# Performance work log

Hardware: AMD Instinct MI355X
Metric: run time of the kernel (lower is better)

## Reference

```python
import jax, jax.numpy as jnp
import numpy as np


def setup_inputs() -> dict:
    key = jax.random.key(0)
    ks = jax.random.split(key, 7)
    B, D, d1, d2, d3 = 256, 256, 1024, 512, 256
    s = lambda f: 1.0 / np.sqrt(f)  # torch nn.Linear-style init scale
    return {
        "x": jax.random.normal(ks[0], (B, D), jnp.float32),
        "W1": jax.random.normal(ks[1], (d1, D), jnp.float32) * s(D),
        "b1": jax.random.normal(ks[2], (d1,), jnp.float32) * s(D),
        "W2": jax.random.normal(ks[3], (d2, d1), jnp.float32) * s(d1),
        "b2": jax.random.normal(ks[4], (d2,), jnp.float32) * s(d1),
        "W3": jax.random.normal(ks[5], (d3, d2), jnp.float32) * s(d2),
        "b3": jax.random.normal(ks[6], (d3,), jnp.float32) * s(d2),
        "k": 10,
    }


def _border_dists(x, W1, b1, W2, b2, W3, b3):
    # Layer 1: pre-activations and boundary distances. For the first layer the
    # effective linear map is W1 itself (shared across the batch).
    z1 = x @ W1.T + b1                                   # [B, d1]
    dist1 = jnp.abs(z1) / jnp.linalg.norm(W1, axis=1)    # [B, d1]
    m1 = (z1 > 0).astype(x.dtype)
    V1 = m1[:, :, None] * W1[None]                       # [B, d1, D] per-instance map after ReLU
    h1 = m1 * z1

    # Layer 2
    z2 = h1 @ W2.T + b2                                  # [B, d2]
    V2 = jnp.einsum('oi,bid->bod', W2, V1)               # [B, d2, D]
    dist2 = jnp.abs(z2) / jnp.linalg.norm(V2, axis=2)
    m2 = (z2 > 0).astype(x.dtype)
    h2 = m2 * z2

    # Layer 3
    z3 = h2 @ W3.T + b3                                  # [B, d3]
    V3 = jnp.einsum('oi,bid->bod', W3, m2[:, :, None] * V2)  # [B, d3, D]
    dist3 = jnp.abs(z3) / jnp.linalg.norm(V3, axis=2)

    return jnp.concatenate([dist1, dist2, dist3], axis=1)  # [B, d1+d2+d3]


def reference(x, W1, b1, W2, b2, W3, b3, k):
    dists = _border_dists(x, W1, b1, W2, b2, W3, b3)
    # smallest-k distances per instance via top_k on negated distances
    neg_top, _ = jax.lax.top_k(-dists, k)                # [B, k]
    return jnp.sum(-neg_top)                             # border-distance loss (scalar)
```

## Files before the change

kernel.cpp:

```cpp
#include <hip/hip_runtime.h>
#include <math.h>
#include <float.h>

#define B   256
#define D   256
#define D1  1024
#define D2  512
#define D3  256
#define NDIST (D1 + D2 + D3)
#define CQ  2.0f

typedef __attribute__((ext_vector_type(8))) short short8;
typedef __attribute__((ext_vector_type(4))) float f32x4;
typedef __attribute__((ext_vector_type(4))) int   i32x4;

__device__ __forceinline__ float waveReduceSum(float v) {
    #pragma unroll
    for (int off = 32; off > 0; off >>= 1)
        v += __shfl_down(v, off, 64);
    return v;
}
__device__ __forceinline__ float waveReduceMax(float v) {
    #pragma unroll
    for (int off = 32; off > 0; off >>= 1)
        v = fmaxf(v, __shfl_down(v, off, 64));
    return v;
}
__device__ __forceinline__ unsigned short f2bf(float f) {
    unsigned int u = __float_as_uint(f);
    u = (u + 0x7FFFu + ((u >> 16) & 1u)) >> 16;
    return (unsigned short)u;
}
__device__ __forceinline__ float bf2f(unsigned short h) {
    return __uint_as_float(((unsigned int)h) << 16);
}
__device__ __forceinline__ void gld16(const void* g, void* l) {
    __builtin_amdgcn_global_load_lds(
        (const __attribute__((address_space(1))) unsigned int*)g,
        (__attribute__((address_space(3))) unsigned int*)l, 16, 0, 0);
}
__device__ __forceinline__ int swz_src(int row, int lane) {
    return ((lane & 3) + ((row >> 1) & 3)) & 3;
}
__device__ __forceinline__ int swz_frag(int row, int quad) {
    return row * 32 + (((quad - ((row >> 1) & 3)) & 3) * 8);
}

__device__ __forceinline__ void split8(const float* p, short8& h8, short8& l8) {
    float4 a = *(const float4*)(p);
    float4 b = *(const float4*)(p + 4);
    float hv[8] = { a.x, a.y, a.z, a.w, b.x, b.y, b.z, b.w };
    #pragma unroll
    for (int q = 0; q < 8; q++) {
        unsigned short hh = f2bf(hv[q]);
        h8[q] = (short)hh;
        l8[q] = (short)f2bf(hv[q] - bf2f(hh));
    }
}

template <int KD, int KL>
__device__ __forceinline__ void mfma3_64(
    const unsigned short* __restrict__ Ahi, const unsigned short* __restrict__ Alo,
    const unsigned short* __restrict__ Bhi, const unsigned short* __restrict__ Blo,
    int m0, int n0, int k0, unsigned short* sm, f32x4 acc[2][2]) {
    int tid = threadIdx.x;
    int l = tid & 63, w = tid >> 6;
    int rsub = l >> 2;
    int quad = l >> 4, l16 = l & 15;
    int wm = (w >> 1) * 32, wn = (w & 1) * 32;
    unsigned short* sAh = sm;
    unsigned short* sAl = sm + 2048;
    unsigned short* sBh = sm + 4096;
    unsigned short* sBl = sm + 6144;
    ptrdiff_t dA = Alo - Ahi, dB = Blo - Bhi;
    int rloc = w * 16 + rsub;
    int c = swz_src(rloc, l);
    const unsigned short* pa = Ahi + (size_t)(m0 + rloc) * KD + k0 + c * 8;
    const unsigned short* pb = Bhi + (size_t)(n0 + rloc) * KD + k0 + c * 8;
    int aoff[2], boff[2];
    #pragma unroll
    for (int mt = 0; mt < 2; mt++) aoff[mt] = swz_frag(wm + mt * 16 + l16, quad);
    #pragma unroll
    for (int nt = 0; nt < 2; nt++) boff[nt] = swz_frag(wn + nt * 16 + l16, quad);
    for (int kk = 0; kk < KL; kk += 32) {
        gld16(pa + kk,      sAh + w * 512);
        gld16(pa + dA + kk, sAl + w * 512);
        gld16(pb + kk,      sBh + w * 512);
        gld16(pb + dB + kk, sBl + w * 512);
        __syncthreads();
        short8 ah[2], al[2], bh[2], bl[2];
        #pragma unroll
        for (int mt = 0; mt < 2; mt++) {
            ah[mt] = *(const short8*)(sAh + aoff[mt]);
            al[mt] = *(const short8*)(sAl + aoff[mt]);
        }
        #pragma unroll
        for (int nt = 0; nt < 2; nt++) {
            bh[nt] = *(const short8*)(sBh + boff[nt]);
            bl[nt] = *(const short8*)(sBl + boff[nt]);
        }
        #pragma unroll
        for (int mt = 0; mt < 2; mt++)
            #pragma unroll
            for (int nt = 0; nt < 2; nt++) {
                acc[mt][nt] = __builtin_amdgcn_mfma_f32_16x16x32_bf16(ah[mt], bh[nt], acc[mt][nt], 0, 0, 0);
                acc[mt][nt] = __builtin_amdgcn_mfma_f32_16x16x32_bf16(ah[mt], bl[nt], acc[mt][nt], 0, 0, 0);
                acc[mt][nt] = __builtin_amdgcn_mfma_f32_16x16x32_bf16(al[mt], bh[nt], acc[mt][nt], 0, 0, 0);
            }
        __syncthreads();
    }
}

__global__ __launch_bounds__(256) void k_l1p(
    const float* __restrict__ x, const float* __restrict__ W1,
    const float* __restrict__ W2, const float* __restrict__ W3,
    const float* __restrict__ b1,
    float* __restrict__ dists, unsigned char* __restrict__ m1q,
    unsigned short* __restrict__ h1hi, unsigned short* __restrict__ h1lo,
    float* __restrict__ zeros, float* __restrict__ outp,
    unsigned short* __restrict__ W2hi, unsigned short* __restrict__ W2lo,
    unsigned short* __restrict__ W3hi, unsigned short* __restrict__ W3lo,
    signed char* __restrict__ W1Ti8, float* __restrict__ saq,
    signed char* __restrict__ W2i8,  float* __restrict__ sbq,
    signed char* __restrict__ W3i8,  float* __restrict__ s3q,
    float* __restrict__ rn1) {
    __shared__ __align__(16) unsigned short sm[8192];
    int blk = blockIdx.x;
    int t = threadIdx.x;

    if (blk < 64) {
        unsigned short* sAh = sm;
        unsigned short* sAl = sm + 2048;
        unsigned short* sBh = sm + 4096;
        unsigned short* sBl = sm + 6144;
        int m0 = (blk & 3) * 64, n0 = (blk >> 2) * 64;
        int l = t & 63, w = t >> 6;
        int rsub = l >> 2;
        int quad = l >> 4, l16 = l & 15;
        int wm = (w >> 1) * 32, wn = (w & 1) * 32;
        int rloc = w * 16 + rsub;
        int c = swz_src(rloc, l);
        const float* pax = x + (size_t)(m0 + rloc) * D + c * 8;
        const float* pbw = W1 + (size_t)(n0 + rloc) * D + c * 8;
        int aoff[2], boff[2];
        #pragma unroll
        for (int mt = 0; mt < 2; mt++) aoff[mt] = swz_frag(wm + mt * 16 + l16, quad);
        #pragma unroll
        for (int nt = 0; nt < 2; nt++) boff[nt] = swz_frag(wn + nt * 16 + l16, quad);
        int wrA = w * 512 + l * 8;
        f32x4 acc[2][2] = {};
        for (int kk = 0; kk < D; kk += 32) {
            short8 ha, la, hb, lb;
            split8(pax + kk, ha, la);
            split8(pbw + kk, hb, lb);
            *(short8*)(sAh + wrA) = ha;
            *(short8*)(sAl + wrA) = la;
            *(short8*)(sBh + wrA) = hb;
            *(short8*)(sBl + wrA) = lb;
            __syncthreads();
            short8 ah[2], al[2], bh[2], bl[2];
            #pragma unroll
            for (int mt = 0; mt < 2; mt++) {
                ah[mt] = *(const short8*)(sAh + aoff[mt]);
                al[mt] = *(const short8*)(sAl + aoff[mt]);
            }
            #pragma unroll
            for (int nt = 0; nt < 2; nt++) {
                bh[nt] = *(const short8*)(sBh + boff[nt]);
                bl[nt] = *(const short8*)(sBl + boff[nt]);
            }
            #pragma unroll
            for (int mt = 0; mt < 2; mt++)
                #pragma unroll
                for (int nt = 0; nt < 2; nt++) {
                    acc[mt][nt] = __builtin_amdgcn_mfma_f32_16x16x32_bf16(ah[mt], bh[nt], acc[mt][nt], 0, 0, 0);
                    acc[mt][nt] = __builtin_amdgcn_mfma_f32_16x16x32_bf16(ah[mt], bl[nt], acc[mt][nt], 0, 0, 0);
                    acc[mt][nt] = __builtin_amdgcn_mfma_f32_16x16x32_bf16(al[mt], bh[nt], acc[mt][nt], 0, 0, 0);
                }
            __syncthreads();
        }
        #pragma unroll
        for (int mt = 0; mt < 2; mt++)
            #pragma unroll
            for (int nt = 0; nt < 2; nt++) {
                int n = n0 + wn + nt * 16 + l16;
                float bv = b1[n];
                #pragma unroll
                for (int r = 0; r < 4; r++) {
                    int m = m0 + wm + mt * 16 + quad * 4 + r;
                    float z = acc[mt][nt][r] + bv;
                    size_t idx = (size_t)m * D1 + n;
                    dists[idx] = fabsf(z);
                    m1q[idx] = (z > 0.f) ? 0xFFu : 0u;
                    float h = z > 0.f ? z : 0.f;
                    unsigned short hh = f2bf(h);
                    h1hi[idx] = hh;
                    h1lo[idx] = f2bf(h - bf2f(hh));
                }
            }
        return;
    }
    if (blk < 448) {
        if (blk == 64 && t == 0) outp[0] = 0.f;
        int i4 = (blk - 64) * 1024 + t * 4;
        *(float4*)(zeros + i4) = make_float4(0.f, 0.f, 0.f, 0.f);
        return;
    }
    if (blk < 480) {
        int ty = t >> 5, tx = t & 31;
        int d = (blk - 448) * 8 + ty;
        float m = 0.f;
        for (int i = tx; i < D1; i += 32) m = fmaxf(m, fabsf(W1[(size_t)i * D + d]));
        #pragma unroll
        for (int off = 16; off > 0; off >>= 1) m = fmaxf(m, __shfl_down(m, off, 32));
        m = __shfl(m, 0, 32);
        m = fmaxf(m, 1e-20f);
        if (tx == 0) saq[d] = m / 127.f;
        float inv = 127.f / m;
        for (int i = tx; i < D1; i += 32) {
            int q = __float2int_rn(W1[(size_t)i * D + d] * inv);
            W1Ti8[(size_t)d * D1 + i] = (signed char)q;
        }
        return;
    }
    if (blk < 608) {
        int o = (blk - 480) * 4 + (t >> 6);
        int l = t & 63;
        const float* row = W2 + (size_t)o * D1;
        float4 v[4];
        #pragma unroll
        for (int jj = 0; jj < 4; jj++) v[jj] = *(const float4*)(row + jj * 256 + l * 4);
        float m = 0.f;
        #pragma unroll
        for (int jj = 0; jj < 4; jj++)
            m = fmaxf(m, fmaxf(fmaxf(fabsf(v[jj].x), fabsf(v[jj].y)),
                               fmaxf(fabsf(v[jj].z), fabsf(v[jj].w))));
        m = waveReduceMax(m);
        m = __shfl(m, 0, 64);
        m = fmaxf(m, 1e-20f);
        if (l == 0) sbq[o] = m / 127.f;
        float inv = 127.f / m;
        #pragma unroll
        for (int jj = 0; jj < 4; jj++) {
            int base = jj * 256 + l * 4;
            int q0 = __float2int_rn(v[jj].x * inv);
            int q1 = __float2int_rn(v[jj].y * inv);
            int q2 = __float2int_rn(v[jj].z * inv);
            int q3 = __float2int_rn(v[jj].w * inv);
            unsigned int pk = (unsigned)(q0 & 255) | ((unsigned)(q1 & 255) << 8) |
                              ((unsigned)(q2 & 255) << 16) | ((unsigned)(q3 & 255) << 24);
            *(unsigned int*)(W2i8 + (size_t)o * D1 + base) = pk;
            ushort4 h, lo;
            h.x = f2bf(v[jj].x); lo.x = f2bf(v[jj].x - bf2f(h.x));
            h.y = f2bf(v[jj].y); lo.y = f2bf(v[jj].y - bf2f(h.y));
            h.z = f2bf(v[jj].z); lo.z = f2bf(v[jj].z - bf2f(h.z));
            h.w = f2bf(v[jj].w); lo.w = f2bf(v[jj].w - bf2f(h.w));
            *(ushort4*)(W2hi + (size_t)o * D1 + base) = h;
            *(ushort4*)(W2lo + (size_t)o * D1 + base) = lo;
        }
        return;
    }
    if (blk < 672) {
        int p = (blk - 608) * 4 + (t >> 6);
        int l = t & 63;
        const float* row = W3 + (size_t)p * D2;
        float4 v[2];
        #pragma unroll
        for (int jj = 0; jj < 2; jj++) v[jj] = *(const float4*)(row + jj * 256 + l * 4);
        float m = 0.f;
        #pragma unroll
        for (int jj = 0; jj < 2; jj++)
            m = fmaxf(m, fmaxf(fmaxf(fabsf(v[jj].x), fabsf(v[jj].y)),
                               fmaxf(fabsf(v[jj].z), fabsf(v[jj].w))));
        m = waveReduceMax(m);
        m = __shfl(m, 0, 64);
        m = fmaxf(m, 1e-20f);
        if (l == 0) s3q[p] = m / 127.f;
        float inv = 127.f / m;
        #pragma unroll
        for (int jj = 0; jj < 2; jj++) {
            int base = jj * 256 + l * 4;
            int q0 = __float2int_rn(v[jj].x * inv);
            int q1 = __float2int_rn(v[jj].y * inv);
            int q2 = __float2int_rn(v[jj].z * inv);
            int q3 = __float2int_rn(v[jj].w * inv);
            unsigned int pk = (unsigned)(q0 & 255) | ((unsigned)(q1 & 255) << 8) |
                              ((unsigned)(q2 & 255) << 16) | ((unsigned)(q3 & 255) << 24);
            *(unsigned int*)(W3i8 + (size_t)p * D2 + base) = pk;
            ushort4 h, lo;
            h.x = f2bf(v[jj].x); lo.x = f2bf(v[jj].x - bf2f(h.x));
            h.y = f2bf(v[jj].y); lo.y = f2bf(v[jj].y - bf2f(h.y));
            h.z = f2bf(v[jj].z); lo.z = f2bf(v[jj].z - bf2f(h.z));
            h.w = f2bf(v[jj].w); lo.w = f2bf(v[jj].w - bf2f(h.w));
            *(ushort4*)(W3hi + (size_t)p * D2 + base) = h;
            *(ushort4*)(W3lo + (size_t)p * D2 + base) = lo;
        }
        return;
    }
    {
        int gw = (blk - 672) * 4 + (t >> 6);
        int lane = t & 63;
        const float* row = W1 + (size_t)gw * D;
        float s = 0.f;
        for (int tt = lane; tt < D; tt += 64) { float v = row[tt]; s += v * v; }
        s = waveReduceSum(s);
        if (lane == 0) rn1[gw] = sqrtf(s);
    }
}

__global__ __launch_bounds__(256, 2) void k_big1(
    const unsigned short* __restrict__ h1hi, const unsigned short* __restrict__ h1lo,
    const unsigned short* __restrict__ W2hi, const unsigned short* __restrict__ W2lo,
    float* __restrict__ z2,
    const signed char* __restrict__ W1Ti8,
    const signed char* __restrict__ W2i8,
    const unsigned char* __restrict__ m1q,
    const float* __restrict__ saq,
    const float* __restrict__ sbq,
    signed char* __restrict__ qV2,
    float* __restrict__ norm2) {
    __shared__ __align__(16) unsigned char smem[67584];
    int bid = blockIdx.x;

    if (bid < 128) {
        unsigned short* sm = (unsigned short*)smem;
        int m0 = (bid & 3) * 64, n0 = ((bid >> 2) & 7) * 64, k0 = (bid >> 5) * 256;
        f32x4 acc[2][2] = {};
        mfma3_64<D1, 256>(h1hi, h1lo, W2hi, W2lo, m0, n0, k0, sm, acc);
        int l = threadIdx.x & 63, w = threadIdx.x >> 6;
        int quad = l >> 4, l16 = l & 15;
        int wm = (w >> 1) * 32, wn = (w & 1) * 32;
        #pragma unroll
        for (int mt = 0; mt < 2; mt++)
            #pragma unroll
            for (int nt = 0; nt < 2; nt++) {
                int n = n0 + wn + nt * 16 + l16;
                #pragma unroll
                for (int r = 0; r < 4; r++) {
                    int m = m0 + wm + mt * 16 + quad * 4 + r;
                    atomicAdd(&z2[(size_t)m * D2 + n], acc[mt][nt][r]);
                }
            }
        return;
    }

    int j = bid - 128;
    int m0 = (j & 1) * 128;
    int o0 = ((j >> 1) & 3) * 128;
    int b0 = (j >> 3) * 2;
    int tid = threadIdx.x;
    int l = tid & 63, w = tid >> 6;
    int quad = l >> 4, l16 = l & 15;
    int wm = (w >> 1) * 64, wn = (w & 1) * 64;
    unsigned char* mbuf = (unsigned char*)smem + 65536;

    *(int2*)(mbuf + tid * 8) = *(const int2*)(m1q + (size_t)b0 * D1 + tid * 8);

    const signed char* pa[4];
    const signed char* pb[4];
    int lrow = l >> 3, ls = l & 7;
    #pragma unroll
    for (int r = 0; r < 4; r++) {
        int row = r * 32 + w * 8 + lrow;
        int c = (ls + (row & 7)) & 7;
        pa[r] = W1Ti8 + (size_t)(m0 + row) * D1 + c * 16;
        pb[r] = W2i8 + (size_t)(o0 + row) * D1 + c * 16;
    }
    int aoff[4][2], boff[4][2];
    #pragma unroll
    for (int mt = 0; mt < 4; mt++) {
        int tr = wm + mt * 16 + l16;
        #pragma unroll
        for (int ks = 0; ks < 2; ks++)
            aoff[mt][ks] = tr * 128 + (((ks * 4 + quad) - (tr & 7)) & 7) * 16;
    }
    #pragma unroll
    for (int nt = 0; nt < 4; nt++) {
        int tr = wn + nt * 16 + l16;
        #pragma unroll
        for (int ks = 0; ks < 2; ks++)
            boff[nt][ks] = tr * 128 + (((ks * 4 + quad) - (tr & 7)) & 7) * 16;
    }

    i32x4 acc[2][4][4];
    #pragma unroll
    for (int g = 0; g < 2; g++)
        #pragma unroll
        for (int i = 0; i < 4; i++)
            #pragma unroll
            for (int jj = 0; jj < 4; jj++) acc[g][i][jj] = (i32x4)0;

    int wr = w * 1024 + l * 16;
    i32x4 sga[4], sgb[4];
    #pragma unroll
    for (int r = 0; r < 4; r++) {
        sga[r] = *(const i32x4*)(pa[r]);
        sgb[r] = *(const i32x4*)(pb[r]);
    }
    {
        signed char* buf0 = (signed char*)smem;
        #pragma unroll
        for (int r = 0; r < 4; r++) {
            *(i32x4*)(buf0 + r * 4096 + wr) = sga[r];
            *(i32x4*)(buf0 + 16384 + r * 4096 + wr) = sgb[r];
        }
    }
    __syncthreads();

    #pragma unroll
    for (int t = 0; t < 8; t++) {
        const signed char* bufc = (const signed char*)smem + ((t & 1) << 15);
        signed char* bufn = (signed char*)smem + (((t + 1) & 1) << 15);
        if (t < 7) {
            int kn = (t + 1) * 128;
            #pragma unroll
            for (int r = 0; r < 4; r++) {
                sga[r] = *(const i32x4*)(pa[r] + kn);
                sgb[r] = *(const i32x4*)(pb[r] + kn);
            }
        }
        const signed char* As = bufc;
        const signed char* Bs = bufc + 16384;
        #pragma unroll
        for (int ks = 0; ks < 2; ks++) {
            i32x4 mva = *(const i32x4*)(mbuf +        t * 128 + ks * 64 + quad * 16);
            i32x4 mvb = *(const i32x4*)(mbuf + 1024 + t * 128 + ks * 64 + quad * 16);
            i32x4 a[4], bq[4];
            #pragma unroll
            for (int mt = 0; mt < 4; mt++)
                a[mt] = *(const i32x4*)(As + aoff[mt][ks]);
            #pragma unroll
            for (int nt = 0; nt < 4; nt++)
                bq[nt] = *(const i32x4*)(Bs + boff[nt][ks]);
            #pragma unroll
            for (int mt = 0; mt < 4; mt++) {
                i32x4 a0 = a[mt] & mva;
                i32x4 a1 = a[mt] & mvb;
                #pragma unroll
                for (int nt = 0; nt < 4; nt++)
                    acc[0][mt][nt] = __builtin_amdgcn_mfma_i32_16x16x64_i8(
                        a0, bq[nt], acc[0][mt][nt], 0, 0, 0);
                #pragma unroll
                for (int nt = 0; nt < 4; nt++)
                    acc[1][mt][nt] = __builtin_amdgcn_mfma_i32_16x16x64_i8(
                        a1, bq[nt], acc[1][mt][nt], 0, 0, 0);
            }
        }
        if (t < 7) {
            #pragma unroll
            for (int r = 0; r < 4; r++) {
                *(i32x4*)(bufn + r * 4096 + wr) = sga[r];
                *(i32x4*)(bufn + 16384 + r * 4096 + wr) = sgb[r];
            }
        }
        __syncthreads();
    }

    float sad[4][4];
    #pragma unroll
    for (int mt = 0; mt < 4; mt++)
        #pragma unroll
        for (int r = 0; r < 4; r++)
            sad[mt][r] = saq[m0 + wm + mt * 16 + quad * 4 + r];
    float sbv[4], sbdq[4];
    #pragma unroll
    for (int nt = 0; nt < 4; nt++) {
        sbv[nt] = sbq[o0 + wn + nt * 16 + l16];
        sbdq[nt] = sbv[nt] * (1.0f / CQ);
    }

    #pragma unroll
    for (int g = 0; g < 2; g++) {
        int bg = b0 + g;
        float nrm[4] = {0.f, 0.f, 0.f, 0.f};
        signed char* qb = qV2 + (size_t)bg * (D * D2);
        #pragma unroll
        for (int mt = 0; mt < 4; mt++) {
            int dbase = m0 + wm + mt * 16 + quad * 4;
            #pragma unroll
            for (int r = 0; r < 4; r++) {
                float sa = sad[mt][r];
                size_t rowoff = (size_t)(dbase + r) * D2;
                #pragma unroll
                for (int nt = 0; nt < 4; nt++) {
                    float tv = (float)acc[g][mt][nt][r];
                    float u = tv * sa;
                    nrm[nt] = fmaf(u, u, nrm[nt]);
                    int qi = __float2int_rn(tv * sbdq[nt]);
                    qi = max(-127, min(127, qi));
                    qb[rowoff + o0 + wn + nt * 16 + l16] = (signed char)qi;
                }
            }
        }
        #pragma unroll
        for (int nt = 0; nt < 4; nt++) {
            float s = nrm[nt] * (sbv[nt] * sbv[nt]);
            s += __shfl_down(s, 32, 64);
            s += __shfl_down(s, 16, 64);
            if (l < 16)
                atomicAdd(&norm2[(size_t)bg * D2 + o0 + wn + nt * 16 + l], s);
        }
    }
}

__global__ __launch_bounds__(256, 2) void k_big2(
    const float* __restrict__ z2,
    const float* __restrict__ b2,
    const unsigned short* __restrict__ W3hi, const unsigned short* __restrict__ W3lo,
    float* __restrict__ z3,
    const signed char* __restrict__ W3i8,
    const signed char* __restrict__ qV2,
    const float* __restrict__ saq,
    const float* __restrict__ s3q,
    float* __restrict__ norm3) {
    __shared__ __align__(16) unsigned char smem[66048];
    int bid = blockIdx.x;
    int tid = threadIdx.x;

    if (bid < 32) {
        unsigned short* sAh = (unsigned short*)smem;
        unsigned short* sAl = sAh + 2048;
        unsigned short* sBh = sAh + 4096;
        unsigned short* sBl = sAh + 6144;
        int m0 = (bid & 3) * 64, n0 = ((bid >> 2) & 3) * 64, k0 = (bid >> 4) * 256;
        int l = tid & 63, w = tid >> 6;
        int rsub = l >> 2;
        int quad = l >> 4, l16 = l & 15;
        int wm = (w >> 1) * 32, wn = (w & 1) * 32;
        int rloc = w * 16 + rsub;
        int c = swz_src(rloc, l);
        const float* pz  = z2 + (size_t)(m0 + rloc) * D2 + k0 + c * 8;
        const float* pbi = b2 + k0 + c * 8;
        const unsigned short* pb = W3hi + (size_t)(n0 + rloc) * D2 + k0 + c * 8;
        ptrdiff_t dB = W3lo - W3hi;
        int aoff[2], boff[2];
        #pragma unroll
        for (int mt = 0; mt < 2; mt++) aoff[mt] = swz_frag(wm + mt * 16 + l16, quad);
        #pragma unroll
        for (int nt = 0; nt < 2; nt++) boff[nt] = swz_frag(wn + nt * 16 + l16, quad);
        int wrA = w * 512 + l * 8;
        f32x4 acc[2][2] = {};
        for (int kk = 0; kk < 256; kk += 32) {
            gld16(pb + kk,      sBh + w * 512);
            gld16(pb + dB + kk, sBl + w * 512);
            float4 za = *(const float4*)(pz + kk);
            float4 zb = *(const float4*)(pz + kk + 4);
            float4 ba = *(const float4*)(pbi + kk);
            float4 bb = *(const float4*)(pbi + kk + 4);
            float hv[8] = { za.x + ba.x, za.y + ba.y, za.z + ba.z, za.w + ba.w,
                            zb.x + bb.x, zb.y + bb.y, zb.z + bb.z, zb.w + bb.w };
            short8 h8, l8;
            #pragma unroll
            for (int q2 = 0; q2 < 8; q2++) {
                float h = hv[q2] > 0.f ? hv[q2] : 0.f;
                unsigned short hh = f2bf(h);
                h8[q2] = (short)hh;
                l8[q2] = (short)f2bf(h - bf2f(hh));
            }
            *(short8*)(sAh + wrA) = h8;
            *(short8*)(sAl + wrA) = l8;
            __syncthreads();
            short8 ah[2], al[2], bh[2], bl[2];
            #pragma unroll
            for (int mt = 0; mt < 2; mt++) {
                ah[mt] = *(const short8*)(sAh + aoff[mt]);
                al[mt] = *(const short8*)(sAl + aoff[mt]);
            }
            #pragma unroll
            for (int nt = 0; nt < 2; nt++) {
                bh[nt] = *(const short8*)(sBh + boff[nt]);
                bl[nt] = *(const short8*)(sBl + boff[nt]);
            }
            #pragma unroll
            for (int mt = 0; mt < 2; mt++)
                #pragma unroll
                for (int nt = 0; nt < 2; nt++) {
                    acc[mt][nt] = __builtin_amdgcn_mfma_f32_16x16x32_bf16(ah[mt], bh[nt], acc[mt][nt], 0, 0, 0);
                    acc[mt][nt] = __builtin_amdgcn_mfma_f32_16x16x32_bf16(ah[mt], bl[nt], acc[mt][nt], 0, 0, 0);
                    acc[mt][nt] = __builtin_amdgcn_mfma_f32_16x16x32_bf16(al[mt], bh[nt], acc[mt][nt], 0, 0, 0);
                }
            __syncthreads();
        }
        #pragma unroll
        for (int mt = 0; mt < 2; mt++)
            #pragma unroll
            for (int nt = 0; nt < 2; nt++) {
                int n = n0 + wn + nt * 16 + l16;
                #pragma unroll
                for (int r = 0; r < 4; r++) {
                    int m = m0 + wm + mt * 16 + quad * 4 + r;
                    atomicAdd(&z3[(size_t)m * D3 + n], acc[mt][nt][r]);
                }
            }
        return;
    }

    int j = bid - 32;
    unsigned char* mbuf = (unsigned char*)smem + 65536;
    int m0 = (j & 1) * 128;
    int n0 = ((j >> 1) & 1) * 128;
    int bc = j >> 2;
    int l = tid & 63, w = tid >> 6;
    int quad = l >> 4, l16 = l & 15;
    int wm = (w >> 1) * 64, wn = (w & 1) * 64;
    const signed char* Bsrc = qV2 + (size_t)bc * (D * D2);

    {
        #pragma unroll
        for (int rr = 0; rr < 2; rr++) {
            int o = tid * 2 + rr;
            float z = z2[(size_t)bc * D2 + o] + b2[o];
            mbuf[o] = (z > 0.f) ? 0xFFu : 0u;
        }
    }

    const signed char* pa[4];
    const signed char* pb[4];
    int lrow = l >> 3, ls = l & 7;
    #pragma unroll
    for (int r = 0; r < 4; r++) {
        int row = r * 32 + w * 8 + lrow;
        int c = (ls + (row & 7)) & 7;
        pa[r] = W3i8 + (size_t)(m0 + row) * D2 + c * 16;
        pb[r] = Bsrc + (size_t)(n0 + row) * D2 + c * 16;
    }
    int aoff[4][2], boff[4][2];
    #pragma unroll
    for (int mt = 0; mt < 4; mt++) {
        int tr = wm + mt * 16 + l16;
        #pragma unroll
        for (int ks = 0; ks < 2; ks++)
            aoff[mt][ks] = tr * 128 + (((ks * 4 + quad) - (tr & 7)) & 7) * 16;
    }
    #pragma unroll
    for (int nt = 0; nt < 4; nt++) {
        int tr = wn + nt * 16 + l16;
        #pragma unroll
        for (int ks = 0; ks < 2; ks++)
            boff[nt][ks] = tr * 128 + (((ks * 4 + quad) - (tr & 7)) & 7) * 16;
    }

    i32x4 acc[4][4];
    #pragma unroll
    for (int i = 0; i < 4; i++)
        #pragma unroll
        for (int jj = 0; jj < 4; jj++) acc[i][jj] = (i32x4)0;

    int wr = w * 1024 + l * 16;
    i32x4 sga[4], sgb[4];
    #pragma unroll
    for (int r = 0; r < 4; r++) {
        sga[r] = *(const i32x4*)(pa[r]);
        sgb[r] = *(const i32x4*)(pb[r]);
    }
    {
        signed char* buf0 = (signed char*)smem;
        #pragma unroll
        for (int r = 0; r < 4; r++) {
            *(i32x4*)(buf0 + r * 4096 + wr) = sga[r];
            *(i32x4*)(buf0 + 16384 + r * 4096 + wr) = sgb[r];
        }
    }
    __syncthreads();

    #pragma unroll
    for (int t = 0; t < 4; t++) {
        const signed char* bufc = (const signed char*)smem + ((t & 1) << 15);
        signed char* bufn = (signed char*)smem + (((t + 1) & 1) << 15);
        if (t < 3) {
            int kn = (t + 1) * 128;
            #pragma unroll
            for (int r = 0; r < 4; r++) {
                sga[r] = *(const i32x4*)(pa[r] + kn);
                sgb[r] = *(const i32x4*)(pb[r] + kn);
            }
        }
        int kk = t * 128;
        const signed char* As = bufc;
        const signed char* Bs = bufc + 16384;
        i32x4 mv0 = *(const i32x4*)(mbuf + kk + quad * 16);
        i32x4 mv1 = *(const i32x4*)(mbuf + kk + 64 + quad * 16);
        #pragma unroll
        for (int ks = 0; ks < 2; ks++) {
            i32x4 mv = ks ? mv1 : mv0;
            i32x4 a[4], bq[4];
            #pragma unroll
            for (int mt = 0; mt < 4; mt++)
                a[mt] = *(const i32x4*)(As + aoff[mt][ks]);
            #pragma unroll
            for (int nt = 0; nt < 4; nt++)
                bq[nt] = (*(const i32x4*)(Bs + boff[nt][ks])) & mv;
            #pragma unroll
            for (int mt = 0; mt < 4; mt++)
                #pragma unroll
                for (int nt = 0; nt < 4; nt++)
                    acc[mt][nt] = __builtin_amdgcn_mfma_i32_16x16x64_i8(
                        a[mt], bq[nt], acc[mt][nt], 0, 0, 0);
        }
        if (t < 3) {
            #pragma unroll
            for (int r = 0; r < 4; r++) {
                *(i32x4*)(bufn + r * 4096 + wr) = sga[r];
                *(i32x4*)(bufn + 16384 + r * 4096 + wr) = sgb[r];
            }
        }
        __syncthreads();
    }

    float saCQ[4];
    #pragma unroll
    for (int nt = 0; nt < 4; nt++)
        saCQ[nt] = saq[n0 + wn + nt * 16 + l16] * CQ;

    #pragma unroll
    for (int mt = 0; mt < 4; mt++)
        #pragma unroll
        for (int r = 0; r < 4; r++) {
            float s = 0.f;
            #pragma unroll
            for (int nt = 0; nt < 4; nt++) {
                float v = (float)acc[mt][nt][r] * saCQ[nt];
                s += v * v;
            }
            s += __shfl_down(s, 8, 64);
            s += __shfl_down(s, 4, 64);
            s += __shfl_down(s, 2, 64);
            s += __shfl_down(s, 1, 64);
            if (l16 == 0) {
                int p = m0 + wm + mt * 16 + quad * 4 + r;
                float s3 = s3q[p];
                atomicAdd(&norm3[(size_t)bc * D3 + p], s * s3 * s3);
            }
        }
}

__global__ __launch_bounds__(256) void k_topk(
    const float* __restrict__ dists,
    const float* __restrict__ rn1,
    const float* __restrict__ z2, const float* __restrict__ b2,
    const float* __restrict__ norm2,
    const float* __restrict__ z3, const float* __restrict__ b3,
    const float* __restrict__ norm3,
    const int* __restrict__ kp, float* __restrict__ outp) {
    int t = threadIdx.x;
    int wv = t >> 6, lane = t & 63;
    int b = blockIdx.x * 4 + wv;
    float lv[28];
    #pragma unroll
    for (int j = 0; j < 16; j++) {
        int n = lane + 64 * j;
        lv[j] = dists[(size_t)b * D1 + n] / rn1[n];
    }
    #pragma unroll
    for (int j = 16; j < 24; j++) {
        int o = lane + 64 * (j - 16);
        float zz = z2[(size_t)b * D2 + o] + b2[o];
        lv[j] = fabsf(zz) / sqrtf(norm2[(size_t)b * D2 + o]);
    }
    #pragma unroll
    for (int j = 24; j < 28; j++) {
        int p = lane + 64 * (j - 24);
        float zz = z3[(size_t)b * D3 + p] + b3[p];
        lv[j] = fabsf(zz) / sqrtf(norm3[(size_t)b * D3 + p]);
    }
    int k = *kp;
    if (k > NDIST) k = NDIST;
    float sum = 0.f;
    for (int it = 0; it < k; it++) {
        float mv = lv[0]; int mj = 0;
        #pragma unroll
        for (int j = 1; j < 28; j++)
            if (lv[j] < mv) { mv = lv[j]; mj = j; }
        unsigned long long key =
            ((unsigned long long)__float_as_uint(mv) << 32) | (unsigned)(lane * 32 + mj);
        #pragma unroll
        for (int off = 1; off < 64; off <<= 1) {
            unsigned long long o = __shfl_xor(key, off, 64);
            if (o < key) key = o;
        }
        sum += __uint_as_float((unsigned)(key >> 32));
        int wl = (int)((key >> 5) & 63u), wj = (int)(key & 31u);
        if (lane == wl) lv[wj] = FLT_MAX;
    }
    if (lane == 0) atomicAdd(outp, sum);
}

extern "C" void kernel_launch(void* const* d_in, const int* in_sizes, int n_in,
                              void* d_out, int out_size, void* d_ws, size_t ws_size,
                              hipStream_t stream) {
    const float* x  = (const float*)d_in[0];
    const float* W1 = (const float*)d_in[1];
    const float* b1 = (const float*)d_in[2];
    const float* W2 = (const float*)d_in[3];
    const float* b2 = (const float*)d_in[4];
    const float* W3 = (const float*)d_in[5];
    const float* b3 = (const float*)d_in[6];
    const int*   kp = (const int*)d_in[7];
    float* outp = (float*)d_out;

    float* fp = (float*)d_ws;
    float* rn1     = fp;                          fp += D1;
    float* dists   = fp;                          fp += (size_t)B * D1;
    float* saq     = fp;                          fp += D;
    float* sbq     = fp;                          fp += D2;
    float* s3q     = fp;                          fp += D3;
    float* z2      = fp;                          fp += (size_t)B * D2;
    float* z3      = fp;                          fp += (size_t)B * D3;
    float* norm2   = fp;                          fp += (size_t)B * D2;
    float* norm3   = fp;                          fp += (size_t)B * D3;
    unsigned short* up = (unsigned short*)fp;
    unsigned short* W2hi  = up;  up += (size_t)D2 * D1;
    unsigned short* W2lo  = up;  up += (size_t)D2 * D1;
    unsigned short* W3hi  = up;  up += (size_t)D3 * D2;
    unsigned short* W3lo  = up;  up += (size_t)D3 * D2;
    unsigned short* h1hi  = up;  up += (size_t)B * D1;
    unsigned short* h1lo  = up;  up += (size_t)B * D1;
    signed char*    cp = (signed char*)up;
    signed char*    W1Ti8 = cp;  cp += (size_t)D * D1;
    signed char*    W2i8  = cp;  cp += (size_t)D2 * D1;
    signed char*    W3i8  = cp;  cp += (size_t)D3 * D2;
    unsigned char*  m1q   = (unsigned char*)cp;  cp += (size_t)B * D1;
    signed char*    qV2   = cp;

    k_l1p<<<928, 256, 0, stream>>>(x, W1, W2, W3, b1,
                                   dists, m1q, h1hi, h1lo,
                                   z2, outp, W2hi, W2lo, W3hi, W3lo,
                                   W1Ti8, saq, W2i8, sbq, W3i8, s3q, rn1);

    k_big1<<<1152, 256, 0, stream>>>(h1hi, h1lo, W2hi, W2lo, z2,
                                     W1Ti8, W2i8, m1q, saq, sbq, qV2, norm2);

    k_big2<<<1056, 256, 0, stream>>>(z2, b2, W3hi, W3lo, z3,
                                     W3i8, qV2, saq, s3q, norm3);

    k_topk<<<B / 4, 256, 0, stream>>>(dists, rn1, z2, b2, norm2, z3, b3, norm3,
                                      kp, outp);
}
```

Before: 170.9 us.

## Use direct global-to-LDS loads with single buffer in int8 V-GEMM kernels

Replaces the register-staged double-buffered LDS pipeline in the int8 MFMA paths of k_big1 and k_big2 with direct global-to-LDS loads (gld16) into a single buffer, synchronised before and after each K step. This halves shared memory use and frees the staging registers, which may allow more resident blocks. k_big2's launch bound drops its min-blocks hint. The cost is losing overlap between the next tile's global loads and the current tile's MFMAs, because each step now waits for its own loads to finish.

```diff
diff --git a/kernel.cpp b/kernel.cpp
--- a/kernel.cpp
+++ b/kernel.cpp
@@ -319,7 +319,7 @@
     const float* __restrict__ sbq,
     signed char* __restrict__ qV2,
     float* __restrict__ norm2) {
-    __shared__ __align__(16) unsigned char smem[67584];
+    __shared__ __align__(16) unsigned char smem[34816];
     int bid = blockIdx.x;
 
     if (bid < 128) {
@@ -345,6 +345,9 @@
     }
 
     int j = bid - 128;
+    signed char* As = (signed char*)smem;
+    signed char* Bs = (signed char*)smem + 16384;
+    unsigned char* mbuf = (unsigned char*)smem + 32768;
     int m0 = (j & 1) * 128;
     int o0 = ((j >> 1) & 3) * 128;
     int b0 = (j >> 3) * 2;
@@ -352,7 +355,6 @@
     int l = tid & 63, w = tid >> 6;
     int quad = l >> 4, l16 = l & 15;
     int wm = (w >> 1) * 64, wn = (w & 1) * 64;
-    unsigned char* mbuf = (unsigned char*)smem + 65536;
 
     *(int2*)(mbuf + tid * 8) = *(const int2*)(m1q + (size_t)b0 * D1 + tid * 8);
 
@@ -390,37 +392,14 @@
             #pragma unroll
             for (int jj = 0; jj < 4; jj++) acc[g][i][jj] = (i32x4)0;
 
-    int wr = w * 1024 + l * 16;
-    i32x4 sga[4], sgb[4];
-    #pragma unroll
-    for (int r = 0; r < 4; r++) {
-        sga[r] = *(const i32x4*)(pa[r]);
-        sgb[r] = *(const i32x4*)(pb[r]);
-    }
-    {
-        signed char* buf0 = (signed char*)smem;
+    for (int t = 0; t < 8; t++) {
+        int kk = t * 128;
         #pragma unroll
         for (int r = 0; r < 4; r++) {
-            *(i32x4*)(buf0 + r * 4096 + wr) = sga[r];
-            *(i32x4*)(buf0 + 16384 + r * 4096 + wr) = sgb[r];
-        }
-    }
-    __syncthreads();
-
-    #pragma unroll
-    for (int t = 0; t < 8; t++) {
-        const signed char* bufc = (const signed char*)smem + ((t & 1) << 15);
-        signed char* bufn = (signed char*)smem + (((t + 1) & 1) << 15);
-        if (t < 7) {
-            int kn = (t + 1) * 128;
-            #pragma unroll
-            for (int r = 0; r < 4; r++) {
-                sga[r] = *(const i32x4*)(pa[r] + kn);
-                sgb[r] = *(const i32x4*)(pb[r] + kn);
-            }
-        }
-        const signed char* As = bufc;
-        const signed char* Bs = bufc + 16384;
+            gld16(pa[r] + kk, As + r * 4096 + w * 1024);
+            gld16(pb[r] + kk, Bs + r * 4096 + w * 1024);
+        }
+        __syncthreads();
         #pragma unroll
         for (int ks = 0; ks < 2; ks++) {
             i32x4 mva = *(const i32x4*)(mbuf +        t * 128 + ks * 64 + quad * 16);
@@ -444,13 +423,6 @@
                 for (int nt = 0; nt < 4; nt++)
                     acc[1][mt][nt] = __builtin_amdgcn_mfma_i32_16x16x64_i8(
                         a1, bq[nt], acc[1][mt][nt], 0, 0, 0);
-            }
-        }
-        if (t < 7) {
-            #pragma unroll
-            for (int r = 0; r < 4; r++) {
-                *(i32x4*)(bufn + r * 4096 + wr) = sga[r];
-                *(i32x4*)(bufn + 16384 + r * 4096 + wr) = sgb[r];
             }
         }
         __syncthreads();
@@ -503,7 +475,7 @@
     }
 }
 
-__global__ __launch_bounds__(256, 2) void k_big2(
+__global__ __launch_bounds__(256) void k_big2(
     const float* __restrict__ z2,
     const float* __restrict__ b2,
     const unsigned short* __restrict__ W3hi, const unsigned short* __restrict__ W3lo,
@@ -513,7 +485,7 @@
     const float* __restrict__ saq,
     const float* __restrict__ s3q,
     float* __restrict__ norm3) {
-    __shared__ __align__(16) unsigned char smem[66048];
+    __shared__ __align__(16) unsigned char smem[33280];
     int bid = blockIdx.x;
     int tid = threadIdx.x;
 
@@ -596,7 +568,9 @@
     }
 
     int j = bid - 32;
-    unsigned char* mbuf = (unsigned char*)smem + 65536;
+    signed char* As = (signed char*)smem;
+    signed char* Bs = (signed char*)smem + 16384;
+    unsigned char* mbuf = (unsigned char*)smem + 32768;
     int m0 = (j & 1) * 128;
     int n0 = ((j >> 1) & 1) * 128;
     int bc = j >> 2;
@@ -613,6 +587,7 @@
             mbuf[o] = (z > 0.f) ? 0xFFu : 0u;
         }
     }
+    __syncthreads();
 
     const signed char* pa[4];
     const signed char* pb[4];
@@ -646,38 +621,13 @@
         #pragma unroll
         for (int jj = 0; jj < 4; jj++) acc[i][jj] = (i32x4)0;
 
-    int wr = w * 1024 + l * 16;
-    i32x4 sga[4], sgb[4];
-    #pragma unroll
-    for (int r = 0; r < 4; r++) {
-        sga[r] = *(const i32x4*)(pa[r]);
-        sgb[r] = *(const i32x4*)(pb[r]);
-    }
-    {
-        signed char* buf0 = (signed char*)smem;
+    for (int kk = 0; kk < D2; kk += 128) {
         #pragma unroll
         for (int r = 0; r < 4; r++) {
-            *(i32x4*)(buf0 + r * 4096 + wr) = sga[r];
-            *(i32x4*)(buf0 + 16384 + r * 4096 + wr) = sgb[r];
-        }
-    }
-    __syncthreads();
-
-    #pragma unroll
-    for (int t = 0; t < 4; t++) {
-        const signed char* bufc = (const signed char*)smem + ((t & 1) << 15);
-        signed char* bufn = (signed char*)smem + (((t + 1) & 1) << 15);
-        if (t < 3) {
-            int kn = (t + 1) * 128;
-            #pragma unroll
-            for (int r = 0; r < 4; r++) {
-                sga[r] = *(const i32x4*)(pa[r] + kn);
-                sgb[r] = *(const i32x4*)(pb[r] + kn);
-            }
-        }
-        int kk = t * 128;
-        const signed char* As = bufc;
-        const signed char* Bs = bufc + 16384;
+            gld16(pa[r] + kk, As + r * 4096 + w * 1024);
+            gld16(pb[r] + kk, Bs + r * 4096 + w * 1024);
+        }
+        __syncthreads();
         i32x4 mv0 = *(const i32x4*)(mbuf + kk + quad * 16);
         i32x4 mv1 = *(const i32x4*)(mbuf + kk + 64 + quad * 16);
         #pragma unroll
@@ -696,13 +646,6 @@
                 for (int nt = 0; nt < 4; nt++)
                     acc[mt][nt] = __builtin_amdgcn_mfma_i32_16x16x64_i8(
                         a[mt], bq[nt], acc[mt][nt], 0, 0, 0);
-        }
-        if (t < 3) {
-            #pragma unroll
-            for (int r = 0; r < 4; r++) {
-                *(i32x4*)(bufn + r * 4096 + wr) = sga[r];
-                *(i32x4*)(bufn + 16384 + r * 4096 + wr) = sgb[r];
-            }
         }
         __syncthreads();
     }
```

After: 161.8 us. 1.06x faster.
